# Optimization experiments

Measured on AMD Instinct MI355X. Metric: run time of the kernel, lower is better.

## Reference

```python
import jax, jax.numpy as jnp
import numpy as np
import math

B, S, D_IN, D, H, L, NC = 4, 2048, 64, 512, 8, 2, 2
DK = D // H
FACTOR = 5
TOPK = min(FACTOR * int(math.log(S)), S)  # 35
EPS = 1e-5


def make_pe():
    # sinusoidal positional encoding [S, D]
    pos = jnp.arange(S, dtype=jnp.float32)[:, None]
    div = jnp.exp(jnp.arange(0, D, 2, dtype=jnp.float32) * (-math.log(10000.0) / D))
    pe = jnp.zeros((S, D), jnp.float32)
    pe = pe.at[:, 0::2].set(jnp.sin(pos * div)).at[:, 1::2].set(jnp.cos(pos * div))
    return pe


def layernorm(x, g, b):
    m = x.mean(-1, keepdims=True)
    v = x.var(-1, keepdims=True)
    return (x - m) / jnp.sqrt(v + EPS) * g + b


def setup_inputs() -> dict:
    key = jax.random.key(0)
    ks = iter(jax.random.split(key, 16))
    def p(shape, s=0.02):
        return jax.random.normal(next(ks), shape, jnp.float32) * s
    return dict(
        x=jax.random.normal(next(ks), (B, S, D_IN), jnp.float32),
        emb_w=p((D_IN, D)), emb_b=jnp.zeros((D,), jnp.float32),
        wq=p((L, D, D)), bq=jnp.zeros((L, D), jnp.float32),
        wk=p((L, D, D)), bk=jnp.zeros((L, D), jnp.float32),
        wv=p((L, D, D)), bv=jnp.zeros((L, D), jnp.float32),
        wo=p((L, D, D)), bo=jnp.zeros((L, D), jnp.float32),
        ff1_w=p((L, D, 4 * D)), ff1_b=jnp.zeros((L, 4 * D), jnp.float32),
        ff2_w=p((L, 4 * D, D)), ff2_b=jnp.zeros((L, D), jnp.float32),
        ln1_g=jnp.ones((L, D), jnp.float32), ln1_b=jnp.zeros((L, D), jnp.float32),
        ln2_g=jnp.ones((L, D), jnp.float32), ln2_b=jnp.zeros((L, D), jnp.float32),
        dec1_w=p((D, D // 2)), dec1_b=jnp.zeros((D // 2,), jnp.float32),
        dec2_w=p((D // 2, NC)), dec2_b=jnp.zeros((NC,), jnp.float32),
    )


def reference(x, emb_w, emb_b, wq, bq, wk, bk, wv, bv, wo, bo,
              ff1_w, ff1_b, ff2_w, ff2_b, ln1_g, ln1_b, ln2_g, ln2_b,
              dec1_w, dec1_b, dec2_w, dec2_b):
    h = x @ emb_w + emb_b + make_pe()[None]  # [B,S,D]
    scale = 1.0 / math.sqrt(DK)
    for i in range(L):
        q = (h @ wq[i] + bq[i]).reshape(B, S, H, DK).transpose(0, 2, 1, 3)
        k = (h @ wk[i] + bk[i]).reshape(B, S, H, DK).transpose(0, 2, 1, 3)
        v = (h @ wv[i] + bv[i]).reshape(B, S, H, DK).transpose(0, 2, 1, 3)
        scores = jnp.einsum('bhqd,bhkd->bhqk', q, k) * scale  # [B,H,S,S]
        top_scores, _ = jax.lax.top_k(scores, TOPK)            # [B,H,S,TOPK]
        attn = jax.nn.softmax(top_scores, axis=-1)
        # NOTE: faithful to source quirk — V sliced to its FIRST TOPK rows,
        # top_indices are discarded by the original module.
        ao = jnp.einsum('bhqk,bhkd->bhqd', attn, v[:, :, :TOPK, :])
        ao = ao.transpose(0, 2, 1, 3).reshape(B, S, D) @ wo[i] + bo[i]
        h = layernorm(h + ao, ln1_g[i], ln1_b[i])
        ff = jax.nn.relu(h @ ff1_w[i] + ff1_b[i]) @ ff2_w[i] + ff2_b[i]
        h = layernorm(h + ff, ln2_g[i], ln2_b[i])
    pooled = h.mean(axis=1)  # AdaptiveAvgPool1d(1) over seq
    out = jax.nn.relu(pooled @ dec1_w + dec1_b) @ dec2_w + dec2_b  # [B,NC]
    return out
```

## Files before the change

kernel.cpp:

```cpp
#include <hip/hip_runtime.h>
#include <cmath>

typedef unsigned short u16;
typedef __attribute__((ext_vector_type(8))) short short8;
typedef __attribute__((ext_vector_type(4))) float float4v;
typedef unsigned short ushort2v __attribute__((ext_vector_type(2)));

#define S_LEN 2048
#define NTOK  8192
#define TOPK  35
#define NT512 ((size_t)NTOK*512)

__device__ __forceinline__ u16 f2b(float f){
  unsigned int x = __float_as_uint(f);
  unsigned int r = (x + 0x7fffu + ((x >> 16) & 1u)) >> 16;
  return (u16)r;
}
__device__ __forceinline__ float b2f(u16 u){
  return __uint_as_float(((unsigned int)u) << 16);
}

__device__ __forceinline__ unsigned key_of(float f){
  unsigned u = (unsigned)f2b(f);
  unsigned m = (u & 0x8000u) ? 0xFFFFu : 0x8000u;
  return (u ^ m) & 0xFFFFu;
}
__device__ __forceinline__ float key_to_f(unsigned key){
  unsigned m = (key & 0x8000u) ? 0x8000u : 0xFFFFu;
  return __uint_as_float(((key ^ m) & 0xFFFFu) << 16);
}
__device__ __forceinline__ unsigned pkmax(unsigned a, unsigned b){
  union { unsigned u; ushort2v v; } x, y, r;
  x.u = a; y.u = b;
  r.v = __builtin_elementwise_max(x.v, y.v);
  return r.u;
}
__device__ __forceinline__ unsigned pkmin(unsigned a, unsigned b){
  union { unsigned u; ushort2v v; } x, y, r;
  x.u = a; y.u = b;
  r.v = __builtin_elementwise_min(x.v, y.v);
  return r.u;
}

__device__ __forceinline__ void bsort128(unsigned &v0, unsigned &v1, int l){
  #pragma unroll
  for (int k = 2; k <= 128; k <<= 1){
    #pragma unroll
    for (int j = k >> 1; j > 0; j >>= 1){
      if (j == 64){
        unsigned hi = pkmax(v0, v1), lo = pkmin(v0, v1);
        v0 = hi; v1 = lo;
      } else {
        unsigned o0 = (unsigned)__shfl_xor((int)v0, j, 64);
        unsigned o1 = (unsigned)__shfl_xor((int)v1, j, 64);
        bool up0 = (((l & k) == 0) != ((l & j) != 0));
        bool up1 = ((((64 + l) & k) == 0) != ((l & j) != 0));
        unsigned hi0 = pkmax(v0, o0), lo0 = pkmin(v0, o0);
        unsigned hi1 = pkmax(v1, o1), lo1 = pkmin(v1, o1);
        v0 = up0 ? hi0 : lo0;
        v1 = up1 ? hi1 : lo1;
      }
    }
  }
}

__device__ __forceinline__ void gload16(const void* g, void* l){
  __builtin_amdgcn_global_load_lds(
      (const __attribute__((address_space(1))) unsigned int*)g,
      (__attribute__((address_space(3))) unsigned int*)l, 16, 0, 0);
}

struct WtArgs {
  const float* wq; const float* wk; const float* wv; const float* wo;
  const float* ff1w; const float* ff2w;
  u16* wt_qkv; u16* wt_wo; u16* wt_ff1; u16* wt_ff2;
};
__global__ void convert_all(WtArgs a){
  __shared__ u16 t[32][33];
  int l = blockIdx.y;
  int tt = blockIdx.x;
  const float* W; u16* Wt; int K, N, tx_, ty_;
  if (tt < 1024){
    int seg = tt >> 8, r = tt & 255;
    tx_ = r & 15; ty_ = r >> 4; K = 512; N = 512;
    if (seg == 0){ W = a.wq + (size_t)l*262144; Wt = a.wt_qkv + (size_t)l*786432; }
    else if (seg == 1){ W = a.wk + (size_t)l*262144; Wt = a.wt_qkv + (size_t)l*786432 + 262144; }
    else if (seg == 2){ W = a.wv + (size_t)l*262144; Wt = a.wt_qkv + (size_t)l*786432 + 524288; }
    else { W = a.wo + (size_t)l*262144; Wt = a.wt_wo + (size_t)l*262144; }
  } else if (tt < 2048){
    int r = tt - 1024;
    tx_ = r & 63; ty_ = r >> 6; K = 512; N = 2048;
    W = a.ff1w + (size_t)l*1048576; Wt = a.wt_ff1 + (size_t)l*1048576;
  } else {
    int r = tt - 2048;
    tx_ = r & 15; ty_ = r >> 4; K = 2048; N = 512;
    W = a.ff2w + (size_t)l*1048576; Wt = a.wt_ff2 + (size_t)l*1048576;
  }
  int k0 = ty_*32, n0 = tx_*32;
  int tx = threadIdx.x, ty = threadIdx.y;
  #pragma unroll
  for (int i = ty; i < 32; i += 8)
    t[i][tx] = f2b(W[(size_t)(k0+i)*N + n0+tx]);
  __syncthreads();
  #pragma unroll
  for (int i = ty; i < 32; i += 8)
    Wt[(size_t)(n0+i)*K + k0+tx] = t[tx][i];
}

__global__ void embed_kernel(const float* __restrict__ x, const float* __restrict__ w,
                             const float* __restrict__ bias, float* __restrict__ h,
                             u16* __restrict__ h16){
  int t = blockIdx.x;
  int tid = threadIdx.x;
  __shared__ float xs[64];
  if (tid < 64) xs[tid] = x[(size_t)t*64 + tid];
  __syncthreads();
  float acc0 = bias[tid];
  float acc1 = bias[tid + 256];
  #pragma unroll 8
  for (int k = 0; k < 64; ++k){
    float xv = xs[k];
    acc0 += xv * w[k*512 + tid];
    acc1 += xv * w[k*512 + tid + 256];
  }
  int s = t & (S_LEN - 1);
  const float neg_ln1e4_over_D = -9.210340371976184f / 512.f;
  int c0 = tid, c1 = tid + 256;
  float a0 = (float)s * expf((float)(c0 & ~1) * neg_ln1e4_over_D);
  float p0 = (c0 & 1) ? cosf(a0) : sinf(a0);
  float a1 = (float)s * expf((float)(c1 & ~1) * neg_ln1e4_over_D);
  float p1 = (c1 & 1) ? cosf(a1) : sinf(a1);
  float v0 = acc0 + p0, v1 = acc1 + p1;
  h[(size_t)t*512 + c0] = v0;  h16[(size_t)t*512 + c0] = f2b(v0);
  h[(size_t)t*512 + c1] = v1;  h16[(size_t)t*512 + c1] = f2b(v1);
}

template<int EPI>
__global__ __launch_bounds__(256) void gemm_mfma(
    const u16* __restrict__ A, int lda, const u16* __restrict__ Bt, int ldb,
    const float* __restrict__ bias0, const float* __restrict__ bias1,
    const float* __restrict__ bias2,
    float* __restrict__ Cf, u16* __restrict__ C16a, u16* __restrict__ C16b,
    float* __restrict__ Cv, int M, int N, int Klen){
  __shared__ __align__(16) u16 As[128*64];
  __shared__ __align__(16) u16 Bs[128*64];
  int tid = threadIdx.x;
  int w = tid >> 6, l = tid & 63, quad = l >> 4, m = l & 15;
  int m0 = blockIdx.y*128, n0 = blockIdx.x*128;
  int mh = (w >> 1)*64, nh = (w & 1)*64;
  float4v acc[4][4];
  #pragma unroll
  for (int i = 0; i < 4; ++i)
    #pragma unroll
    for (int j = 0; j < 4; ++j) acc[i][j] = (float4v){0.f,0.f,0.f,0.f};

  for (int kt = 0; kt < Klen; kt += 64){
    #pragma unroll
    for (int c = 0; c < 4; ++c){
      int g = c*256 + tid;
      int row = g >> 3, sc = g & 7, dc = sc ^ (row & 7);
      gload16(A  + (size_t)(m0+row)*lda + kt + dc*8, As + (size_t)g*8);
      gload16(Bt + (size_t)(n0+row)*ldb + kt + dc*8, Bs + (size_t)g*8);
    }
    __syncthreads();
    #pragma unroll
    for (int kk = 0; kk < 2; ++kk){
      short8 af[4], bf[4];
      #pragma unroll
      for (int i = 0; i < 4; ++i){
        int dcx = kk*4 + quad;
        int ra = mh + i*16 + m;
        af[i] = *(const short8*)(As + (size_t)(ra*8 + (dcx ^ (ra & 7)))*8);
        int rb = nh + i*16 + m;
        bf[i] = *(const short8*)(Bs + (size_t)(rb*8 + (dcx ^ (rb & 7)))*8);
      }
      #pragma unroll
      for (int i = 0; i < 4; ++i)
        #pragma unroll
        for (int j = 0; j < 4; ++j)
          acc[i][j] = __builtin_amdgcn_mfma_f32_16x16x32_bf16(af[i], bf[j], acc[i][j], 0, 0, 0);
    }
    __syncthreads();
  }

  #pragma unroll
  for (int i = 0; i < 4; ++i){
    #pragma unroll
    for (int j = 0; j < 4; ++j){
      int col = n0 + nh + j*16 + m;
      #pragma unroll
      for (int r = 0; r < 4; ++r){
        int row = m0 + mh + i*16 + quad*4 + r;
        float v = acc[i][j][r];
        if (EPI == 0){
          Cf[(size_t)row*N + col] = v + bias0[col];
        } else if (EPI == 1){
          C16a[(size_t)row*N + col] = f2b(fmaxf(v + bias0[col], 0.f));
        } else {
          int sel = col >> 9, n5 = col & 511;
          const float* bp = (sel == 0) ? bias0 : (sel == 1) ? bias1 : bias2;
          float vv = v + bp[n5];
          int d = n5 & 63, hh = n5 >> 6;
          int b = row >> 11, s = row & 2047;
          size_t idx = (((size_t)(b*8 + hh))*2048 + s)*64 + d;
          if (sel == 0)      C16a[idx] = f2b(vv);
          else if (sel == 1) C16b[idx] = f2b(vv);
          else               Cv[idx]  = vv;
        }
      }
    }
  }
}

__global__ __launch_bounds__(512, 8) void attn_mfma_topk(
    const u16* __restrict__ qb16, const u16* __restrict__ kb16,
    const float* __restrict__ vb, u16* __restrict__ aob16){
  __shared__ unsigned pr[8*1024];
  int tid  = threadIdx.x;
  int w    = tid >> 6, l = tid & 63;
  int quad = l >> 4,  m = l & 15;
  int bh = blockIdx.y;
  int q0 = blockIdx.x * 16;

  const u16* Qp = qb16 + ((size_t)bh*2048 + q0 + m)*64 + quad*8;
  short8 a0 = *(const short8*)Qp;
  short8 a1 = *(const short8*)(Qp + 32);

  const u16* Kbase = kb16 + (size_t)bh*2048*64;
  unsigned sc[32];
  int swz = (quad & 1) << 4;
  #pragma unroll
  for (int hlf = 0; hlf < 2; ++hlf){
    #pragma unroll
    for (int kt = 0; kt < 8; ++kt){
      int lk = w*128 + kt*16;
      const u16* Kp = Kbase + (size_t)(hlf*1024 + lk + m)*64 + quad*8;
      short8 b0 = *(const short8*)Kp;
      short8 b1 = *(const short8*)(Kp + 32);
      float4v acc = {0.f, 0.f, 0.f, 0.f};
      acc = __builtin_amdgcn_mfma_f32_16x16x32_bf16(a0, b0, acc, 0, 0, 0);
      acc = __builtin_amdgcn_mfma_f32_16x16x32_bf16(a1, b1, acc, 0, 0, 0);
      #pragma unroll
      for (int c = 0; c < 2; ++c){
        unsigned lo = key_of(acc[2*c]);
        unsigned hi = key_of(acc[2*c+1]);
        pr[(quad*2 + c)*1024 + ((lk + m) ^ swz)] = lo | (hi << 16);
      }
    }
    __syncthreads();
    const uint4* p4 = (const uint4*)(pr + w*1024);
    #pragma unroll
    for (int j = 0; j < 4; ++j){
      uint4 v4 = p4[j*64 + l];
      sc[hlf*16 + j*4+0] = v4.x; sc[hlf*16 + j*4+1] = v4.y;
      sc[hlf*16 + j*4+2] = v4.z; sc[hlf*16 + j*4+3] = v4.w;
    }
    if (hlf == 0) __syncthreads();
  }

  unsigned* row = &pr[w*1024];

  unsigned m1 = pkmax(sc[0], sc[1]);
  unsigned m2 = pkmin(sc[0], sc[1]);
  #pragma unroll
  for (int i = 2; i < 32; ++i){
    unsigned v = sc[i];
    unsigned nm1 = pkmax(m1, v);
    m2 = pkmax(m2, pkmin(m1, v));
    m1 = nm1;
  }

  unsigned mA1 = m1 & 0xFFFFu, mB1 = m1 >> 16;
  unsigned mA2 = m2 & 0xFFFFu, mB2 = m2 >> 16;
  unsigned tA = 0, tB = 0;
  #pragma unroll
  for (int bit = 15; bit >= 0; --bit){
    unsigned cA = tA | (1u << bit);
    unsigned cB = tB | (1u << bit);
    int nA = __popcll(__ballot(mA1 >= cA)) + __popcll(__ballot(mA2 >= cA));
    int nB = __popcll(__ballot(mB1 >= cB)) + __popcll(__ballot(mB2 >= cB));
    if (nA >= TOPK) tA = cA;
    if (nB >= TOPK) tB = cB;
  }
  unsigned TT = (tA - 1) | ((tB - 1) << 16);

  unsigned mask = 0;
  #pragma unroll
  for (int i = 0; i < 32; ++i){
    mask |= (pkmax(sc[i], TT) != TT) ? (1u << i) : 0u;
  }
  int cnt = __popc(mask);

  int pre = cnt;
  #pragma unroll
  for (int off = 1; off < 64; off <<= 1){
    int n = __shfl_up(pre, off, 64);
    if (l >= off) pre += n;
  }
  pre -= cnt;

  #pragma unroll
  for (int i = 0; i < 32; ++i){
    if (mask & (1u << i)){
      int p = pre++;
      if (p < 128) row[p] = sc[i];
    }
  }
  int tot = __shfl(pre, 63, 64);

  unsigned c0 = (l < tot)      ? row[l]      : 0u;
  unsigned c1 = (64 + l < tot) ? row[64 + l] : 0u;

  const float* Vb = vb + (size_t)bh*2048*64 + l;
  float vreg[TOPK];
  #pragma unroll
  for (int r = 0; r < TOPK; ++r) vreg[r] = Vb[(size_t)r*64];

  bsort128(c0, c1, l);

  unsigned top0 = (unsigned)__shfl((int)c0, 0, 64);
  float mAf = key_to_f(top0 & 0xFFFFu) * 0.125f;
  float mBf = key_to_f(top0 >> 16)     * 0.125f;
  float tvA = key_to_f(c0 & 0xFFFFu)   * 0.125f;
  float tvB = key_to_f(c0 >> 16)       * 0.125f;
  float wAv = (l < TOPK) ? __expf(tvA - mAf) : 0.f;
  float wBv = (l < TOPK) ? __expf(tvB - mBf) : 0.f;

  float dA = wAv, dB = wBv;
  #pragma unroll
  for (int off = 32; off > 0; off >>= 1){
    dA += __shfl_xor(dA, off, 64);
    dB += __shfl_xor(dB, off, 64);
  }

  float2* wls = (float2*)(row + 128);
  if (l < TOPK) wls[l] = make_float2(wAv, wBv);

  float accA = 0.f, accB = 0.f;
  #pragma unroll
  for (int r = 0; r < TOPK; ++r){
    float2 wv = wls[r];
    float vv = vreg[r];
    accA += wv.x * vv;
    accB += wv.y * vv;
  }
  accA *= __builtin_amdgcn_rcpf(dA);
  accB *= __builtin_amdgcn_rcpf(dB);

  int b = bh >> 3, hh = bh & 7;
  int sA = q0 + w*2;
  aob16[(((size_t)(b*2048 + sA))*8 + hh)*64 + l]     = f2b(accA);
  aob16[(((size_t)(b*2048 + sA + 1))*8 + hh)*64 + l] = f2b(accB);
}

__global__ void resid_ln_kernel(float* __restrict__ h, const float* __restrict__ t,
                                const float* __restrict__ g, const float* __restrict__ b,
                                u16* __restrict__ h16){
  int tok = blockIdx.x;
  int tid = threadIdx.x;
  size_t base = (size_t)tok * 512;
  float x0 = h[base + tid]       + t[base + tid];
  float x1 = h[base + tid + 256] + t[base + tid + 256];
  __shared__ float red[8];
  int wid = tid >> 6, lane = tid & 63;

  float s = x0 + x1;
  #pragma unroll
  for (int off = 32; off > 0; off >>= 1) s += __shfl_xor(s, off, 64);
  if (lane == 0) red[wid] = s;
  __syncthreads();
  float mean = (red[0] + red[1] + red[2] + red[3]) * (1.f/512.f);

  float d0 = x0 - mean, d1 = x1 - mean;
  float sq = d0*d0 + d1*d1;
  #pragma unroll
  for (int off = 32; off > 0; off >>= 1) sq += __shfl_xor(sq, off, 64);
  if (lane == 0) red[4 + wid] = sq;
  __syncthreads();
  float var = (red[4] + red[5] + red[6] + red[7]) * (1.f/512.f);
  float inv = rsqrtf(var + 1e-5f);
  float o0 = d0 * inv * g[tid]       + b[tid];
  float o1 = d1 * inv * g[tid + 256] + b[tid + 256];
  h[base + tid]         = o0;  h16[base + tid]       = f2b(o0);
  h[base + tid + 256]   = o1;  h16[base + tid + 256] = f2b(o1);
}

__global__ void pool_zero(float* __restrict__ pooled){
  pooled[blockIdx.x*512 + threadIdx.x] = 0.f;
}
__global__ void pool_kernel(const float* __restrict__ h, float* __restrict__ pooled){
  int c = blockIdx.x * 256 + threadIdx.x;
  int b = blockIdx.y;
  int s0 = blockIdx.z * 64;
  const float* p = h + ((size_t)b * 2048 + s0) * 512 + c;
  float acc = 0.f;
  #pragma unroll 8
  for (int s = 0; s < 64; ++s) acc += p[(size_t)s * 512];
  atomicAdd(&pooled[b*512 + c], acc * (1.f/2048.f));
}

__global__ void decoder_kernel(const float* __restrict__ pooled,
                               const float* __restrict__ w1, const float* __restrict__ b1,
                               const float* __restrict__ w2, const float* __restrict__ b2,
                               float* __restrict__ out){
  __shared__ float ps[4][512];
  __shared__ float hid[4][256];
  int tid = threadIdx.x;
  for (int i = tid; i < 2048; i += 256) ps[i >> 9][i & 511] = pooled[i];
  __syncthreads();
  float bb = b1[tid];
  for (int b = 0; b < 4; ++b){
    float acc = bb;
    for (int k = 0; k < 512; ++k) acc += ps[b][k] * w1[k*256 + tid];
    hid[b][tid] = fmaxf(acc, 0.f);
  }
  __syncthreads();
  if (tid < 8){
    int b = tid >> 1, c = tid & 1;
    float acc = b2[c];
    for (int j = 0; j < 256; ++j) acc += hid[b][j] * w2[j*2 + c];
    out[b*2 + c] = acc;
  }
}

extern "C" void kernel_launch(void* const* d_in, const int* in_sizes, int n_in,
                              void* d_out, int out_size, void* d_ws, size_t ws_size,
                              hipStream_t stream){
  const float* x     = (const float*)d_in[0];
  const float* emb_w = (const float*)d_in[1];
  const float* emb_b = (const float*)d_in[2];
  const float* wq    = (const float*)d_in[3];
  const float* bq    = (const float*)d_in[4];
  const float* wk    = (const float*)d_in[5];
  const float* bk    = (const float*)d_in[6];
  const float* wv    = (const float*)d_in[7];
  const float* bv    = (const float*)d_in[8];
  const float* wo    = (const float*)d_in[9];
  const float* bo    = (const float*)d_in[10];
  const float* ff1w  = (const float*)d_in[11];
  const float* ff1b  = (const float*)d_in[12];
  const float* ff2w  = (const float*)d_in[13];
  const float* ff2b  = (const float*)d_in[14];
  const float* ln1g  = (const float*)d_in[15];
  const float* ln1b  = (const float*)d_in[16];
  const float* ln2g  = (const float*)d_in[17];
  const float* ln2b  = (const float*)d_in[18];
  const float* d1w   = (const float*)d_in[19];
  const float* d1b   = (const float*)d_in[20];
  const float* d2w   = (const float*)d_in[21];
  const float* d2b   = (const float*)d_in[22];

  float* h      = (float*)d_ws;
  float* tmp    = h + NT512;
  u16*   u      = (u16*)(tmp + NT512);
  u16*   h16    = u;
  u16*   q16    = u + NT512;
  u16*   k16    = u + 2*NT512;
  float* vb     = (float*)(u + 3*NT512);
  u16*   ff16   = q16;
  u16*   aob16  = (u16*)(vb + NT512);
  u16*   wt     = aob16 + NT512;
  u16*   wt_qkv = wt;
  u16*   wt_wo  = wt_qkv + (size_t)2*1536*512;
  u16*   wt_ff1 = wt_wo  + (size_t)2*512*512;
  u16*   wt_ff2 = wt_ff1 + (size_t)2*2048*512;
  float* pooled = (float*)(wt_ff2 + (size_t)2*512*2048);

  WtArgs wa{wq, wk, wv, wo, ff1w, ff2w, wt_qkv, wt_wo, wt_ff1, wt_ff2};
  convert_all<<<dim3(3072, 2), dim3(32, 8), 0, stream>>>(wa);

  embed_kernel<<<NTOK, 256, 0, stream>>>(x, emb_w, emb_b, h, h16);

  for (int l = 0; l < 2; ++l){
    gemm_mfma<2><<<dim3(12, 64), 256, 0, stream>>>(
        h16, 512, wt_qkv + (size_t)l*1536*512, 512,
        bq + l*512, bk + l*512, bv + l*512,
        nullptr, q16, k16, vb, NTOK, 1536, 512);

    attn_mfma_topk<<<dim3(128, 32), 512, 0, stream>>>(q16, k16, vb, aob16);

    gemm_mfma<0><<<dim3(4, 64), 256, 0, stream>>>(
        aob16, 512, wt_wo + (size_t)l*512*512, 512,
        bo + l*512, nullptr, nullptr,
        tmp, nullptr, nullptr, nullptr, NTOK, 512, 512);
    resid_ln_kernel<<<NTOK, 256, 0, stream>>>(h, tmp, ln1g + l*512, ln1b + l*512, h16);

    gemm_mfma<1><<<dim3(16, 64), 256, 0, stream>>>(
        h16, 512, wt_ff1 + (size_t)l*2048*512, 512,
        ff1b + l*2048, nullptr, nullptr,
        nullptr, ff16, nullptr, nullptr, NTOK, 2048, 512);

    gemm_mfma<0><<<dim3(4, 64), 256, 0, stream>>>(
        ff16, 2048, wt_ff2 + (size_t)l*512*2048, 2048,
        ff2b + l*512, nullptr, nullptr,
        tmp, nullptr, nullptr, nullptr, NTOK, 512, 2048);
    resid_ln_kernel<<<NTOK, 256, 0, stream>>>(h, tmp, ln2g + l*512, ln2b + l*512, h16);
  }

  pool_zero<<<4, 512, 0, stream>>>(pooled);
  pool_kernel<<<dim3(2, 4, 32), 256, 0, stream>>>(h, pooled);
  decoder_kernel<<<1, 256, 0, stream>>>(pooled, d1w, d1b, d2w, d2b, (float*)d_out);
}
```

Before: 745.5 us.

## Swizzle workgroup order for XCDs, prefetch K tiles, vectorize layernorm accesses

Remaps block indices in the GEMM and attention kernels so that consecutive workgroups sharing data land on the same XCD, aiming for better L2 reuse across the MI355X chiplets. The attention score loop is flattened into 16 steps and software-pipelined, loading the next K tile while the current MFMA runs. The serial prefix counter in top-k compaction is replaced with a popcount-based position. The residual layernorm kernel switches to float2 loads and stores and packed bf16 writes. These changes cost extra index arithmetic and register pressure, and the remap assumes grid sizes divisible by 8.

```diff
diff --git a/kernel.cpp b/kernel.cpp
--- a/kernel.cpp
+++ b/kernel.cpp
@@ -146,7 +146,11 @@
   __shared__ __align__(16) u16 Bs[128*64];
   int tid = threadIdx.x;
   int w = tid >> 6, l = tid & 63, quad = l >> 4, m = l & 15;
-  int m0 = blockIdx.y*128, n0 = blockIdx.x*128;
+  int gx = gridDim.x;
+  int orig = blockIdx.y * gx + blockIdx.x;
+  int nwg  = gx * gridDim.y;
+  int tt   = (orig & 7) * (nwg >> 3) + (orig >> 3);
+  int m0 = (tt / gx) * 128, n0 = (tt % gx) * 128;
   int mh = (w >> 1)*64, nh = (w & 1)*64;
   float4v acc[4][4];
   #pragma unroll
@@ -219,8 +223,10 @@
   int tid  = threadIdx.x;
   int w    = tid >> 6, l = tid & 63;
   int quad = l >> 4,  m = l & 15;
-  int bh = blockIdx.y;
-  int q0 = blockIdx.x * 16;
+  int orig = blockIdx.y * 128 + blockIdx.x;
+  int t4   = ((orig & 7) << 9) | (orig >> 3);
+  int bh   = t4 >> 7;
+  int q0   = (t4 & 127) << 4;
 
   const u16* Qp = qb16 + ((size_t)bh*2048 + q0 + m)*64 + quad*8;
   short8 a0 = *(const short8*)Qp;
@@ -229,33 +235,46 @@
   const u16* Kbase = kb16 + (size_t)bh*2048*64;
   unsigned sc[32];
   int swz = (quad & 1) << 4;
-  #pragma unroll
-  for (int hlf = 0; hlf < 2; ++hlf){
+  const u16* kp0 = Kbase + (size_t)(w*128 + m)*64 + quad*8;
+  const uint4* p4 = (const uint4*)(pr + w*1024);
+
+  short8 cb0 = *(const short8*)kp0;
+  short8 cb1 = *(const short8*)(kp0 + 32);
+  #pragma unroll
+  for (int t = 0; t < 16; ++t){
+    short8 nb0, nb1;
+    if (t < 15){
+      int tn = t + 1;
+      const u16* np = kp0 + (size_t)(((tn >> 3) << 10) + ((tn & 7) << 4))*64;
+      nb0 = *(const short8*)np;
+      nb1 = *(const short8*)(np + 32);
+    }
+    float4v acc = {0.f, 0.f, 0.f, 0.f};
+    acc = __builtin_amdgcn_mfma_f32_16x16x32_bf16(a0, cb0, acc, 0, 0, 0);
+    acc = __builtin_amdgcn_mfma_f32_16x16x32_bf16(a1, cb1, acc, 0, 0, 0);
+    int lk = (w << 7) + ((t & 7) << 4);
     #pragma unroll
-    for (int kt = 0; kt < 8; ++kt){
-      int lk = w*128 + kt*16;
-      const u16* Kp = Kbase + (size_t)(hlf*1024 + lk + m)*64 + quad*8;
-      short8 b0 = *(const short8*)Kp;
-      short8 b1 = *(const short8*)(Kp + 32);
-      float4v acc = {0.f, 0.f, 0.f, 0.f};
-      acc = __builtin_amdgcn_mfma_f32_16x16x32_bf16(a0, b0, acc, 0, 0, 0);
-      acc = __builtin_amdgcn_mfma_f32_16x16x32_bf16(a1, b1, acc, 0, 0, 0);
+    for (int c = 0; c < 2; ++c){
+      unsigned lo = key_of(acc[2*c]);
+      unsigned hi = key_of(acc[2*c+1]);
+      pr[(quad*2 + c)*1024 + ((lk + m) ^ swz)] = lo | (hi << 16);
+    }
+    cb0 = nb0; cb1 = nb1;
+    if (t == 7){
+      __syncthreads();
       #pragma unroll
-      for (int c = 0; c < 2; ++c){
-        unsigned lo = key_of(acc[2*c]);
-        unsigned hi = key_of(acc[2*c+1]);
-        pr[(quad*2 + c)*1024 + ((lk + m) ^ swz)] = lo | (hi << 16);
+      for (int j = 0; j < 4; ++j){
+        uint4 v4 = p4[j*64 + l];
+        sc[j*4+0] = v4.x; sc[j*4+1] = v4.y; sc[j*4+2] = v4.z; sc[j*4+3] = v4.w;
       }
-    }
-    __syncthreads();
-    const uint4* p4 = (const uint4*)(pr + w*1024);
-    #pragma unroll
-    for (int j = 0; j < 4; ++j){
-      uint4 v4 = p4[j*64 + l];
-      sc[hlf*16 + j*4+0] = v4.x; sc[hlf*16 + j*4+1] = v4.y;
-      sc[hlf*16 + j*4+2] = v4.z; sc[hlf*16 + j*4+3] = v4.w;
-    }
-    if (hlf == 0) __syncthreads();
+      __syncthreads();
+    }
+  }
+  __syncthreads();
+  #pragma unroll
+  for (int j = 0; j < 4; ++j){
+    uint4 v4 = p4[j*64 + l];
+    sc[16+j*4+0] = v4.x; sc[16+j*4+1] = v4.y; sc[16+j*4+2] = v4.z; sc[16+j*4+3] = v4.w;
   }
 
   unsigned* row = &pr[w*1024];
@@ -302,11 +321,11 @@
   #pragma unroll
   for (int i = 0; i < 32; ++i){
     if (mask & (1u << i)){
-      int p = pre++;
+      int p = pre + __popc(mask & ((1u << i) - 1u));
       if (p < 128) row[p] = sc[i];
     }
   }
-  int tot = __shfl(pre, 63, 64);
+  int tot = __shfl(pre + cnt, 63, 64);
 
   unsigned c0 = (l < tot)      ? row[l]      : 0u;
   unsigned c1 = (64 + l < tot) ? row[64 + l] : 0u;
@@ -358,9 +377,11 @@
                                 u16* __restrict__ h16){
   int tok = blockIdx.x;
   int tid = threadIdx.x;
-  size_t base = (size_t)tok * 512;
-  float x0 = h[base + tid]       + t[base + tid];
-  float x1 = h[base + tid + 256] + t[base + tid + 256];
+  size_t base2 = (size_t)tok * 256;
+  float2 hv = ((const float2*)h)[base2 + tid];
+  float2 tv = ((const float2*)t)[base2 + tid];
+  float x0 = hv.x + tv.x;
+  float x1 = hv.y + tv.y;
   __shared__ float red[8];
   int wid = tid >> 6, lane = tid & 63;
 
@@ -379,10 +400,12 @@
   __syncthreads();
   float var = (red[4] + red[5] + red[6] + red[7]) * (1.f/512.f);
   float inv = rsqrtf(var + 1e-5f);
-  float o0 = d0 * inv * g[tid]       + b[tid];
-  float o1 = d1 * inv * g[tid + 256] + b[tid + 256];
-  h[base + tid]         = o0;  h16[base + tid]       = f2b(o0);
-  h[base + tid + 256]   = o1;  h16[base + tid + 256] = f2b(o1);
+  float2 gv = ((const float2*)g)[tid];
+  float2 bv = ((const float2*)b)[tid];
+  float o0 = d0 * inv * gv.x + bv.x;
+  float o1 = d1 * inv * gv.y + bv.y;
+  ((float2*)h)[base2 + tid] = make_float2(o0, o1);
+  ((unsigned*)h16)[base2 + tid] = (unsigned)f2b(o0) | ((unsigned)f2b(o1) << 16);
 }
 
 __global__ void pool_zero(float* __restrict__ pooled){
```

Measured after the change: 724.6 us. -2.8%, faster.
